# Kernel tuning notes

Hardware: AMD Instinct MI355X
Metric: run time of the kernel (lower is better)

Reference implementation:

```python
import jax, jax.numpy as jnp
import numpy as np

B, T = 8, 30000
DIM = 3
HID = 128          # hidden_dim
CD = 128           # c_dim
R = 64             # plane_resolution
NB = 5             # n_blocks


def setup_inputs() -> dict:
    key = jax.random.key(0)
    ks = jax.random.split(key, 10)
    points = jax.random.uniform(ks[0], (B, T, DIM), dtype=jnp.float32)
    index_xz = jax.random.randint(ks[1], (B, T), 0, R * R, dtype=jnp.int32)
    index_xy = jax.random.randint(ks[2], (B, T), 0, R * R, dtype=jnp.int32)
    index_yz = jax.random.randint(ks[3], (B, T), 0, R * R, dtype=jnp.int32)
    s_in = 1.0 / np.sqrt(DIM)
    s_h2 = 1.0 / np.sqrt(2 * HID)
    s_h = 1.0 / np.sqrt(HID)
    fc_pos_w = jax.random.normal(ks[4], (DIM, 2 * HID), jnp.float32) * s_in
    fc_pos_b = jnp.zeros((2 * HID,), jnp.float32)
    fc0_w = jax.random.normal(ks[5], (NB, 2 * HID, HID), jnp.float32) * s_h2
    fc0_b = jnp.zeros((NB, HID), jnp.float32)
    fc1_w = jax.random.normal(ks[6], (NB, HID, HID), jnp.float32) * s_h
    fc1_b = jnp.zeros((NB, HID), jnp.float32)
    sc_w = jax.random.normal(ks[7], (NB, 2 * HID, HID), jnp.float32) * s_h2
    fc_c_w = jax.random.normal(ks[8], (HID, CD), jnp.float32) * s_h
    fc_c_b = jnp.zeros((CD,), jnp.float32)
    return dict(points=points, index_xz=index_xz, index_xy=index_xy, index_yz=index_yz,
                fc_pos_w=fc_pos_w, fc_pos_b=fc_pos_b, fc0_w=fc0_w, fc0_b=fc0_b,
                fc1_w=fc1_w, fc1_b=fc1_b, sc_w=sc_w, fc_c_w=fc_c_w, fc_c_b=fc_c_b)


def _resnet_block(x, w0, b0, w1, b1, ws):
    # ResnetBlockFC: fc_0(relu(x)) -> fc_1(relu(net)); shortcut is bias-free Linear
    net = jax.nn.relu(x) @ w0 + b0
    dx = jax.nn.relu(net) @ w1 + b1
    return x @ ws + dx


def _pool_max_gather(feat, idx):
    # scatter_max per batch into R*R bins, then gather back per-point
    def per(f, i):  # f: [T, C], i: [T]
        seg = jax.ops.segment_max(f, i, num_segments=R * R)  # [R2, C]
        return seg[i]
    return jax.vmap(per)(feat, idx)


def _plane_mean(c, idx):
    # scatter_mean of c [B, T, CD] into [B, CD, R, R] plane features
    def per(f, i):
        s = jax.ops.segment_sum(f, i, num_segments=R * R)  # [R2, CD]
        cnt = jax.ops.segment_sum(jnp.ones((f.shape[0],), f.dtype), i, num_segments=R * R)
        return s / jnp.maximum(cnt, 1.0)[:, None]
    m = jax.vmap(per)(c, idx)  # [B, R2, CD]
    return jnp.transpose(m, (0, 2, 1)).reshape(c.shape[0], CD, R, R)


def reference(points, index_xz, index_xy, index_yz, fc_pos_w, fc_pos_b,
              fc0_w, fc0_b, fc1_w, fc1_b, sc_w, fc_c_w, fc_c_b):
    idxs = (index_xz, index_xy, index_yz)
    net = points @ fc_pos_w + fc_pos_b                    # [B, T, 2*HID]
    net = _resnet_block(net, fc0_w[0], fc0_b[0], fc1_w[0], fc1_b[0], sc_w[0])  # [B, T, HID]
    for i in range(1, NB):
        pooled = sum(_pool_max_gather(net, idx) for idx in idxs)  # pool_local sums over plane keys
        net = jnp.concatenate([net, pooled], axis=2)      # [B, T, 2*HID]
        net = _resnet_block(net, fc0_w[i], fc0_b[i], fc1_w[i], fc1_b[i], sc_w[i])
    c = net @ fc_c_w + fc_c_b                             # [B, T, CD]
    # fea dict {'xz','xy','yz'} returned as a stacked array [3, B, CD, R, R]
    return jnp.stack([_plane_mean(c, index_xz), _plane_mean(c, index_xy), _plane_mean(c, index_yz)], axis=0)
```

## Files before the change

kernel.cpp:

```cpp
#include <hip/hip_runtime.h>
#include <float.h>

#define BATCH 8
#define TPTS 30000
#define NPR 30016
#define HID 128
#define R2 4096
#define NPTS (BATCH * TPTS)
#define PB 64
#define XS 264
#define HS 136

typedef __attribute__((ext_vector_type(8))) short short8;
typedef __attribute__((ext_vector_type(4))) short short4v;
typedef __attribute__((ext_vector_type(4))) float f32x4;

__device__ __forceinline__ short f2bf(float f) {
    unsigned u = __float_as_uint(f);
    u += 0x7fff + ((u >> 16) & 1);
    return (short)(u >> 16);
}
__device__ __forceinline__ float bf2f(unsigned short u) {
    return __uint_as_float(((unsigned)u) << 16);
}
__device__ __forceinline__ unsigned relu2(unsigned u) {
    unsigned sm = u & 0x80008000u;
    unsigned d  = sm - (sm >> 15);
    return u & ~d;
}
__device__ __forceinline__ short8 relu8(short8 v) {
    union { short8 s; unsigned u[4]; } a;
    a.s = v;
#pragma unroll
    for (int i = 0; i < 4; ++i) a.u[i] = relu2(a.u[i]);
    return a.s;
}

__global__ void k_fill4(float4* p, float v, int n4) {
    int i = blockIdx.x * blockDim.x + threadIdx.x;
    if (i < n4) p[i] = make_float4(v, v, v, v);
}

__global__ __launch_bounds__(256) void k_prep(
    const float* __restrict__ fc0w, const float* __restrict__ fc1w, const float* __restrict__ scw,
    const float* __restrict__ fccw,
    short* __restrict__ Wt0, short* __restrict__ Wts, short* __restrict__ Wt1,
    short* __restrict__ Wtc)
{
    int i = blockIdx.x * 256 + threadIdx.x;
    if (i < 5 * 128 * 256) {
        int r = i >> 15;
        int c = (i >> 8) & 127;
        int k = i & 255;
        Wt0[i] = f2bf(fc0w[(r * 256 + k) * 128 + c]);
        Wts[i] = f2bf(scw [(r * 256 + k) * 128 + c]);
    }
    if (i < 5 * 128 * 128) {
        int r = i >> 14;
        int c = (i >> 7) & 127;
        int k = i & 127;
        Wt1[i] = f2bf(fc1w[(r * 128 + k) * 128 + c]);
    }
    if (i < 128 * 128) {
        int c = (i >> 7) & 127;
        int k = i & 127;
        Wtc[i] = f2bf(fccw[k * 128 + c]);
    }
}

__global__ void k_hist(const int* __restrict__ i0, const int* __restrict__ i1,
                       const int* __restrict__ i2, int* __restrict__ hist)
{
    int t = blockIdx.x * 256 + threadIdx.x;
    if (t >= NPTS) return;
    int b = t / TPTS;
    atomicAdd(&hist[(0 * BATCH + b) * R2 + i0[t]], 1);
    atomicAdd(&hist[(1 * BATCH + b) * R2 + i1[t]], 1);
    atomicAdd(&hist[(2 * BATCH + b) * R2 + i2[t]], 1);
}

__global__ __launch_bounds__(256) void k_scan(const int* __restrict__ hist,
                                              int* __restrict__ starts, int* __restrict__ cursor)
{
    int pb = blockIdx.x;
    const int* h = hist + pb * R2;
    int tid = threadIdx.x;
    __shared__ int part[257];
    int loc[16]; int s = 0;
    int base = tid * 16;
#pragma unroll
    for (int q = 0; q < 16; ++q) { loc[q] = s; s += h[base + q]; }
    part[tid + 1] = s;
    __syncthreads();
    if (tid == 0) {
        part[0] = 0;
        for (int i = 1; i <= 256; ++i) part[i] += part[i - 1];
    }
    __syncthreads();
    int off = part[tid];
#pragma unroll
    for (int q = 0; q < 16; ++q) {
        int v = off + loc[q];
        starts[pb * 4097 + base + q] = v;
        cursor[pb * R2 + base + q] = v;
    }
    if (tid == 255) starts[pb * 4097 + 4096] = part[256];
}

__global__ void k_scatter(const int* __restrict__ i0, const int* __restrict__ i1,
                          const int* __restrict__ i2, int* __restrict__ cursor,
                          unsigned short* __restrict__ order)
{
    int t = blockIdx.x * 256 + threadIdx.x;
    if (t >= NPTS) return;
    int b = t / TPTS;
    int tt = t - b * TPTS;
    int s0 = atomicAdd(&cursor[(0 * BATCH + b) * R2 + i0[t]], 1);
    order[(0 * BATCH + b) * TPTS + s0] = (unsigned short)tt;
    int s1 = atomicAdd(&cursor[(1 * BATCH + b) * R2 + i1[t]], 1);
    order[(1 * BATCH + b) * TPTS + s1] = (unsigned short)tt;
    int s2 = atomicAdd(&cursor[(2 * BATCH + b) * R2 + i2[t]], 1);
    order[(2 * BATCH + b) * TPTS + s2] = (unsigned short)tt;
}

__global__ __launch_bounds__(256) void k_poolmax(
    const short* __restrict__ net, const int* __restrict__ starts,
    const unsigned short* __restrict__ order, short* __restrict__ seg)
{
    int b = blockIdx.x;
    int plane = blockIdx.y >> 10;
    int bin = (blockIdx.y & 1023) * 4 + (threadIdx.x >> 6);
    int pb = plane * BATCH + b;
    int lane = threadIdx.x & 63;
    int s = starts[pb * 4097 + bin], e = starts[pb * 4097 + bin + 1];
    if (s == e) return;
    const unsigned short* ord = order + pb * TPTS;
    float vx = -FLT_MAX, vy = -FLT_MAX;
    for (int i = s; i < e; ++i) {
        int t = b * NPR + ord[i];
        unsigned u = *(const unsigned*)(net + t * HID + lane * 2);
        vx = fmaxf(vx, bf2f((unsigned short)(u & 0xFFFF)));
        vy = fmaxf(vy, bf2f((unsigned short)(u >> 16)));
    }
    unsigned o = ((unsigned short)f2bf(vx)) | (((unsigned)(unsigned short)f2bf(vy)) << 16);
    *(unsigned*)(seg + (pb * R2 + bin) * HID + lane * 2) = o;
}

__global__ __launch_bounds__(256) void k_poolmean(
    const short* __restrict__ net, const int* __restrict__ starts,
    const unsigned short* __restrict__ order, short* __restrict__ meanb)
{
    int b = blockIdx.x;
    int plane = blockIdx.y >> 10;
    int bin = (blockIdx.y & 1023) * 4 + (threadIdx.x >> 6);
    int pb = plane * BATCH + b;
    int lane = threadIdx.x & 63;
    int s = starts[pb * 4097 + bin], e = starts[pb * 4097 + bin + 1];
    const unsigned short* ord = order + pb * TPTS;
    float vx = 0.f, vy = 0.f;
    for (int i = s; i < e; ++i) {
        int t = b * NPR + ord[i];
        unsigned u = *(const unsigned*)(net + t * HID + lane * 2);
        vx += bf2f((unsigned short)(u & 0xFFFF));
        vy += bf2f((unsigned short)(u >> 16));
    }
    float inv = 1.f / fmaxf((float)(e - s), 1.f);
    unsigned o = ((unsigned short)f2bf(vx * inv)) | (((unsigned)(unsigned short)f2bf(vy * inv)) << 16);
    *(unsigned*)(meanb + (pb * R2 + bin) * HID + lane * 2) = o;
}

__device__ __forceinline__ void resnet_body(
    short* xs, const float* b0s, const float* b1s,
    const short* __restrict__ Wt0r, const short* __restrict__ Wtsr,
    const short* __restrict__ Wt1r, short* __restrict__ net_out, int t0)
{
    int tid = threadIdx.x;
    int lane = tid & 63;
    int wave = tid >> 6;
    int n    = lane & 15;
    int quad = lane >> 4;
    int ch0  = wave * 32;

    f32x4 accS[2][4] = {};
    f32x4 accF[2][4] = {};
    for (int ks = 0; ks < 8; ++ks) {
        int ko = ks * 32 + quad * 8;
        short8 aS[2], aF[2];
#pragma unroll
        for (int c = 0; c < 2; ++c) {
            int row = ch0 + c * 16 + n;
            aS[c] = *(const short8*)(Wtsr + row * 256 + ko);
            aF[c] = *(const short8*)(Wt0r + row * 256 + ko);
        }
#pragma unroll
        for (int p = 0; p < 4; ++p) {
            short8 bX = *(const short8*)(xs + (p * 16 + n) * XS + ko);
            short8 bR = relu8(bX);
#pragma unroll
            for (int c = 0; c < 2; ++c) {
                accS[c][p] = __builtin_amdgcn_mfma_f32_16x16x32_bf16(aS[c], bX, accS[c][p], 0, 0, 0);
                accF[c][p] = __builtin_amdgcn_mfma_f32_16x16x32_bf16(aF[c], bR, accF[c][p], 0, 0, 0);
            }
        }
    }
    __syncthreads();

    short* h = xs;
#pragma unroll
    for (int c = 0; c < 2; ++c) {
        int chb = ch0 + c * 16 + quad * 4;
#pragma unroll
        for (int p = 0; p < 4; ++p) {
            int pt = p * 16 + n;
            short4v hv;
#pragma unroll
            for (int r = 0; r < 4; ++r)
                hv[r] = f2bf(fmaxf(accF[c][p][r] + b0s[chb + r], 0.f));
            *(short4v*)&h[pt * HS + chb] = hv;
        }
    }
    __syncthreads();

    for (int ks = 0; ks < 4; ++ks) {
        int ko = ks * 32 + quad * 8;
        short8 a1[2];
#pragma unroll
        for (int c = 0; c < 2; ++c)
            a1[c] = *(const short8*)(Wt1r + (ch0 + c * 16 + n) * 128 + ko);
#pragma unroll
        for (int p = 0; p < 4; ++p) {
            short8 bh = *(const short8*)&h[(p * 16 + n) * HS + ko];
#pragma unroll
            for (int c = 0; c < 2; ++c)
                accS[c][p] = __builtin_amdgcn_mfma_f32_16x16x32_bf16(a1[c], bh, accS[c][p], 0, 0, 0);
        }
    }
    __syncthreads();

#pragma unroll
    for (int c = 0; c < 2; ++c) {
        int chb = ch0 + c * 16 + quad * 4;
#pragma unroll
        for (int p = 0; p < 4; ++p) {
            int pt = p * 16 + n;
            short4v o;
#pragma unroll
            for (int r = 0; r < 4; ++r)
                o[r] = f2bf(accS[c][p][r] + b1s[chb + r]);
            *(short4v*)&h[pt * HS + chb] = o;
        }
    }
    __syncthreads();

    int pr = tid >> 4, l8 = (tid & 15) * 8;
#pragma unroll
    for (int it = 0; it < 4; ++it) {
        int p = it * 16 + pr;
        *(short8*)(net_out + (t0 + p) * HID + l8) = *(const short8*)&h[p * HS + l8];
    }
}

__global__ __launch_bounds__(256, 4) void k_mblock0(
    const float* __restrict__ pts, const float* __restrict__ Wp, const float* __restrict__ bp,
    const short* __restrict__ Wt0, const short* __restrict__ Wts, const short* __restrict__ Wt1,
    const float* __restrict__ b0, const float* __restrict__ b1, short* __restrict__ net)
{
    __shared__ short xs[PB * XS];
    __shared__ float b0s[HID], b1s[HID];
    int tid = threadIdx.x;
    int b  = blockIdx.x;
    int r0 = blockIdx.y * PB;
    if (tid < 128) { b0s[tid] = b0[tid]; b1s[tid] = b1[tid]; }

    int j = tid & 127, half = tid >> 7;
    int col = half * 128 + j;
    float w0 = Wp[col], w1 = Wp[256 + col], w2 = Wp[512 + col];
    float bb = bp[col];
    for (int p = 0; p < PB; ++p) {
        int tt = r0 + p; if (tt > TPTS - 1) tt = TPTS - 1;
        const float* pp = pts + (b * TPTS + tt) * 3;
        float v = fmaf(pp[2], w2, fmaf(pp[1], w1, fmaf(pp[0], w0, bb)));
        xs[p * XS + col] = f2bf(v);
    }
    __syncthreads();
    resnet_body(xs, b0s, b1s, Wt0, Wts, Wt1, net, b * NPR + r0);
}

__global__ __launch_bounds__(256, 4) void k_mblock(
    const short* __restrict__ net_in, const short* __restrict__ seg,
    const int* __restrict__ i0, const int* __restrict__ i1, const int* __restrict__ i2,
    const short* __restrict__ Wt0, const short* __restrict__ Wts, const short* __restrict__ Wt1,
    const float* __restrict__ b0, const float* __restrict__ b1, short* __restrict__ net_out)
{
    __shared__ short xs[PB * XS];
    __shared__ float b0s[HID], b1s[HID];
    int tid = threadIdx.x;
    int b  = blockIdx.x;
    int r0 = blockIdx.y * PB;
    if (tid < 128) { b0s[tid] = b0[tid]; b1s[tid] = b1[tid]; }

    int pr = tid >> 4;
    int l8 = (tid & 15) * 8;
#pragma unroll
    for (int it = 0; it < 4; ++it) {
        int p = it * 16 + pr;
        int tt = r0 + p;
        int ttc = tt > TPTS - 1 ? TPTS - 1 : tt;
        int ib = b * TPTS + ttc;
        int a0 = i0[ib], a1 = i1[ib], a2 = i2[ib];
        *(short8*)&xs[p * XS + l8] = *(const short8*)(net_in + (b * NPR + tt) * HID + l8);
        short8 s0 = *(const short8*)(seg + ((0 * BATCH + b) * R2 + a0) * HID + l8);
        short8 s1 = *(const short8*)(seg + ((1 * BATCH + b) * R2 + a1) * HID + l8);
        short8 s2 = *(const short8*)(seg + ((2 * BATCH + b) * R2 + a2) * HID + l8);
        short8 pv;
#pragma unroll
        for (int r = 0; r < 8; ++r)
            pv[r] = f2bf(bf2f((unsigned short)s0[r]) + bf2f((unsigned short)s1[r]) + bf2f((unsigned short)s2[r]));
        *(short8*)&xs[p * XS + 128 + l8] = pv;
    }
    __syncthreads();
    resnet_body(xs, b0s, b1s, Wt0, Wts, Wt1, net_out, b * NPR + r0);
}

__global__ __launch_bounds__(256) void k_gemmout(
    const short* __restrict__ meanb, const short* __restrict__ Wtc, const float* __restrict__ bc,
    const int* __restrict__ starts, float* __restrict__ out)
{
    __shared__ short bs[64 * HS];
    __shared__ float tile[128 * 66];
    __shared__ float bcs[HID];
    __shared__ int   flg[64];
    int tid = threadIdx.x;
    int b = blockIdx.x;
    int plane = blockIdx.y >> 6;
    int pb = plane * BATCH + b;
    int bin0 = (blockIdx.y & 63) * 64;

    if (tid < 128) bcs[tid] = bc[tid];
    if (tid < 64)  flg[tid] = (starts[pb * 4097 + bin0 + tid + 1] > starts[pb * 4097 + bin0 + tid]);
    for (int c8 = tid; c8 < 1024; c8 += 256) {
        int p = c8 >> 4, l = (c8 & 15) * 8;
        *(short8*)&bs[p * HS + l] = *(const short8*)(meanb + (pb * R2 + bin0 + p) * HID + l);
    }
    __syncthreads();

    int lane = tid & 63, wave = tid >> 6;
    int n = lane & 15, quad = lane >> 4;
    int ch0 = wave * 32;
    f32x4 acc[2][4] = {};
    for (int ks = 0; ks < 4; ++ks) {
        int ko = ks * 32 + quad * 8;
        short8 a[2];
#pragma unroll
        for (int c = 0; c < 2; ++c)
            a[c] = *(const short8*)(Wtc + (ch0 + c * 16 + n) * 128 + ko);
#pragma unroll
        for (int p = 0; p < 4; ++p) {
            short8 bh = *(const short8*)&bs[(p * 16 + n) * HS + ko];
#pragma unroll
            for (int c = 0; c < 2; ++c)
                acc[c][p] = __builtin_amdgcn_mfma_f32_16x16x32_bf16(a[c], bh, acc[c][p], 0, 0, 0);
        }
    }
#pragma unroll
    for (int c = 0; c < 2; ++c) {
        int chb = ch0 + c * 16 + quad * 4;
#pragma unroll
        for (int p = 0; p < 4; ++p) {
            int bin = p * 16 + n;
#pragma unroll
            for (int r = 0; r < 4; ++r)
                tile[(chb + r) * 66 + bin] = acc[c][p][r] + bcs[chb + r];
        }
    }
    __syncthreads();

    for (int c4 = tid; c4 < 2048; c4 += 256) {
        int ch = c4 >> 4, b4 = (c4 & 15) * 4;
        float4 o;
        o.x = flg[b4 + 0] ? tile[ch * 66 + b4 + 0] : 0.f;
        o.y = flg[b4 + 1] ? tile[ch * 66 + b4 + 1] : 0.f;
        o.z = flg[b4 + 2] ? tile[ch * 66 + b4 + 2] : 0.f;
        o.w = flg[b4 + 3] ? tile[ch * 66 + b4 + 3] : 0.f;
        *(float4*)(out + (pb * 128 + ch) * R2 + bin0 + b4) = o;
    }
}

extern "C" void kernel_launch(void* const* d_in, const int* in_sizes, int n_in,
                              void* d_out, int out_size, void* d_ws, size_t ws_size,
                              hipStream_t stream) {
    const float* pts  = (const float*)d_in[0];
    const int*   ixz  = (const int*)d_in[1];
    const int*   ixy  = (const int*)d_in[2];
    const int*   iyz  = (const int*)d_in[3];
    const float* Wp   = (const float*)d_in[4];
    const float* bp   = (const float*)d_in[5];
    const float* fc0w = (const float*)d_in[6];
    const float* fc0b = (const float*)d_in[7];
    const float* fc1w = (const float*)d_in[8];
    const float* fc1b = (const float*)d_in[9];
    const float* scw  = (const float*)d_in[10];
    const float* Wc   = (const float*)d_in[11];
    const float* bc   = (const float*)d_in[12];
    float* out = (float*)d_out;

    short* Wt0 = (short*)d_ws;
    short* Wts = Wt0 + 163840;
    short* Wt1 = Wts + 163840;
    short* Wtc = Wt1 + 81920;
    short* net  = Wtc + 16384;
    short* segb = net + 30736384;
    int* hist   = (int*)(segb + 12582912);
    int* starts = hist + 98304;
    unsigned short* order = (unsigned short*)(starts + 98328);

    k_prep<<<dim3(640), 256, 0, stream>>>(fc0w, fc1w, scw, Wc, Wt0, Wts, Wt1, Wtc);
    k_fill4<<<dim3(96), 256, 0, stream>>>((float4*)hist, 0.f, 98304 / 4);
    k_hist<<<dim3((NPTS + 255) / 256), 256, 0, stream>>>(ixz, ixy, iyz, hist);
    k_scan<<<dim3(24), 256, 0, stream>>>(hist, starts, hist);
    k_scatter<<<dim3((NPTS + 255) / 256), 256, 0, stream>>>(ixz, ixy, iyz, hist, order);

    k_mblock0<<<dim3(8, NPR / PB), 256, 0, stream>>>(pts, Wp, bp, Wt0, Wts, Wt1, fc0b, fc1b, net);

    for (int r = 1; r < 5; ++r) {
        k_poolmax<<<dim3(8, 3 * R2 / 4), 256, 0, stream>>>(net, starts, order, segb);
        k_mblock<<<dim3(8, NPR / PB), 256, 0, stream>>>(
            net, segb, ixz, ixy, iyz,
            Wt0 + r * 32768, Wts + r * 32768, Wt1 + r * 16384,
            fc0b + r * 128, fc1b + r * 128, net);
    }

    k_poolmean<<<dim3(8, 3 * R2 / 4), 256, 0, stream>>>(net, starts, order, segb);
    k_gemmout<<<dim3(8, 3 * 64), 256, 0, stream>>>(segb, Wtc, bc, starts, out);
}
```

Baseline: 993.0 us.

## Unroll pooling gathers, write resnet output directly, vectorize fc_pos, hoist index loads

Unrolls the pool-max and pool-mean gather loops by four so that several independent row loads are in flight per thread. Removes the final shared-memory staging and its two barriers in the resnet body, writing bf16 results straight to global memory in 8-byte pieces. Reworks the fc_pos prologue so each thread handles one point and writes 16-byte vectors to LDS. Hoists the plane index loads in k_mblock ahead of the gather loop. The direct global stores are narrower and less coalesced than the previous 16-byte row copies.

```diff
diff --git a/kernel.cpp b/kernel.cpp
--- a/kernel.cpp
+++ b/kernel.cpp
@@ -135,10 +135,23 @@
     int s = starts[pb * 4097 + bin], e = starts[pb * 4097 + bin + 1];
     if (s == e) return;
     const unsigned short* ord = order + pb * TPTS;
+    const short* nb = net + (size_t)b * NPR * HID + lane * 2;
     float vx = -FLT_MAX, vy = -FLT_MAX;
-    for (int i = s; i < e; ++i) {
-        int t = b * NPR + ord[i];
-        unsigned u = *(const unsigned*)(net + t * HID + lane * 2);
+    int i = s;
+    for (; i + 4 <= e; i += 4) {
+        unsigned u0 = *(const unsigned*)(nb + (int)ord[i + 0] * HID);
+        unsigned u1 = *(const unsigned*)(nb + (int)ord[i + 1] * HID);
+        unsigned u2 = *(const unsigned*)(nb + (int)ord[i + 2] * HID);
+        unsigned u3 = *(const unsigned*)(nb + (int)ord[i + 3] * HID);
+        vx = fmaxf(fmaxf(vx, bf2f((unsigned short)(u0 & 0xFFFF))),
+                   fmaxf(bf2f((unsigned short)(u1 & 0xFFFF)),
+                         fmaxf(bf2f((unsigned short)(u2 & 0xFFFF)), bf2f((unsigned short)(u3 & 0xFFFF)))));
+        vy = fmaxf(fmaxf(vy, bf2f((unsigned short)(u0 >> 16))),
+                   fmaxf(bf2f((unsigned short)(u1 >> 16)),
+                         fmaxf(bf2f((unsigned short)(u2 >> 16)), bf2f((unsigned short)(u3 >> 16)))));
+    }
+    for (; i < e; ++i) {
+        unsigned u = *(const unsigned*)(nb + (int)ord[i] * HID);
         vx = fmaxf(vx, bf2f((unsigned short)(u & 0xFFFF)));
         vy = fmaxf(vy, bf2f((unsigned short)(u >> 16)));
     }
@@ -157,10 +170,21 @@
     int lane = threadIdx.x & 63;
     int s = starts[pb * 4097 + bin], e = starts[pb * 4097 + bin + 1];
     const unsigned short* ord = order + pb * TPTS;
+    const short* nb = net + (size_t)b * NPR * HID + lane * 2;
     float vx = 0.f, vy = 0.f;
-    for (int i = s; i < e; ++i) {
-        int t = b * NPR + ord[i];
-        unsigned u = *(const unsigned*)(net + t * HID + lane * 2);
+    int i = s;
+    for (; i + 4 <= e; i += 4) {
+        unsigned u0 = *(const unsigned*)(nb + (int)ord[i + 0] * HID);
+        unsigned u1 = *(const unsigned*)(nb + (int)ord[i + 1] * HID);
+        unsigned u2 = *(const unsigned*)(nb + (int)ord[i + 2] * HID);
+        unsigned u3 = *(const unsigned*)(nb + (int)ord[i + 3] * HID);
+        vx += (bf2f((unsigned short)(u0 & 0xFFFF)) + bf2f((unsigned short)(u1 & 0xFFFF)))
+            + (bf2f((unsigned short)(u2 & 0xFFFF)) + bf2f((unsigned short)(u3 & 0xFFFF)));
+        vy += (bf2f((unsigned short)(u0 >> 16)) + bf2f((unsigned short)(u1 >> 16)))
+            + (bf2f((unsigned short)(u2 >> 16)) + bf2f((unsigned short)(u3 >> 16)));
+    }
+    for (; i < e; ++i) {
+        unsigned u = *(const unsigned*)(nb + (int)ord[i] * HID);
         vx += bf2f((unsigned short)(u & 0xFFFF));
         vy += bf2f((unsigned short)(u >> 16));
     }
@@ -235,7 +259,6 @@
                 accS[c][p] = __builtin_amdgcn_mfma_f32_16x16x32_bf16(a1[c], bh, accS[c][p], 0, 0, 0);
         }
     }
-    __syncthreads();
 
 #pragma unroll
     for (int c = 0; c < 2; ++c) {
@@ -247,16 +270,8 @@
 #pragma unroll
             for (int r = 0; r < 4; ++r)
                 o[r] = f2bf(accS[c][p][r] + b1s[chb + r]);
-            *(short4v*)&h[pt * HS + chb] = o;
-        }
-    }
-    __syncthreads();
-
-    int pr = tid >> 4, l8 = (tid & 15) * 8;
-#pragma unroll
-    for (int it = 0; it < 4; ++it) {
-        int p = it * 16 + pr;
-        *(short8*)(net_out + (t0 + p) * HID + l8) = *(const short8*)&h[p * HS + l8];
+            *(short4v*)(net_out + (t0 + pt) * HID + chb) = o;
+        }
     }
 }
 
@@ -272,15 +287,22 @@
     int r0 = blockIdx.y * PB;
     if (tid < 128) { b0s[tid] = b0[tid]; b1s[tid] = b1[tid]; }
 
-    int j = tid & 127, half = tid >> 7;
-    int col = half * 128 + j;
-    float w0 = Wp[col], w1 = Wp[256 + col], w2 = Wp[512 + col];
-    float bb = bp[col];
-    for (int p = 0; p < PB; ++p) {
-        int tt = r0 + p; if (tt > TPTS - 1) tt = TPTS - 1;
-        const float* pp = pts + (b * TPTS + tt) * 3;
-        float v = fmaf(pp[2], w2, fmaf(pp[1], w1, fmaf(pp[0], w0, bb)));
-        xs[p * XS + col] = f2bf(v);
+    int pt = tid >> 2;
+    int sub = tid & 3;
+    int tt = r0 + pt; if (tt > TPTS - 1) tt = TPTS - 1;
+    const float* pp = pts + (b * TPTS + tt) * 3;
+    float px = pp[0], py = pp[1], pz = pp[2];
+#pragma unroll
+    for (int c8 = 0; c8 < 8; ++c8) {
+        int col0 = sub * 64 + c8 * 8;
+        short8 v8;
+#pragma unroll
+        for (int r = 0; r < 8; ++r) {
+            int col = col0 + r;
+            float v = fmaf(pz, Wp[512 + col], fmaf(py, Wp[256 + col], fmaf(px, Wp[col], bp[col])));
+            v8[r] = f2bf(v);
+        }
+        *(short8*)&xs[pt * XS + col0] = v8;
     }
     __syncthreads();
     resnet_body(xs, b0s, b1s, Wt0, Wts, Wt1, net, b * NPR + r0);
@@ -301,17 +323,22 @@
 
     int pr = tid >> 4;
     int l8 = (tid & 15) * 8;
+    int a0[4], a1[4], a2[4];
+#pragma unroll
+    for (int it = 0; it < 4; ++it) {
+        int tt = r0 + it * 16 + pr;
+        int ttc = tt > TPTS - 1 ? TPTS - 1 : tt;
+        int ib = b * TPTS + ttc;
+        a0[it] = i0[ib]; a1[it] = i1[ib]; a2[it] = i2[ib];
+    }
 #pragma unroll
     for (int it = 0; it < 4; ++it) {
         int p = it * 16 + pr;
         int tt = r0 + p;
-        int ttc = tt > TPTS - 1 ? TPTS - 1 : tt;
-        int ib = b * TPTS + ttc;
-        int a0 = i0[ib], a1 = i1[ib], a2 = i2[ib];
         *(short8*)&xs[p * XS + l8] = *(const short8*)(net_in + (b * NPR + tt) * HID + l8);
-        short8 s0 = *(const short8*)(seg + ((0 * BATCH + b) * R2 + a0) * HID + l8);
-        short8 s1 = *(const short8*)(seg + ((1 * BATCH + b) * R2 + a1) * HID + l8);
-        short8 s2 = *(const short8*)(seg + ((2 * BATCH + b) * R2 + a2) * HID + l8);
+        short8 s0 = *(const short8*)(seg + ((0 * BATCH + b) * R2 + a0[it]) * HID + l8);
+        short8 s1 = *(const short8*)(seg + ((1 * BATCH + b) * R2 + a1[it]) * HID + l8);
+        short8 s2 = *(const short8*)(seg + ((2 * BATCH + b) * R2 + a2[it]) * HID + l8);
         short8 pv;
 #pragma unroll
         for (int r = 0; r < 8; ++r)
```

Result: faster. 933.3 us (-6.0%).
